# Kernel tuning notes

Hardware: AMD Instinct MI355X
Metric: run time of the kernel (lower is better)

Reference implementation:

```python
import jax, jax.numpy as jnp
import numpy as np

NEG = -1e30  # safe log-space -inf (avoids nan grads from true -inf in logaddexp)


def _ctc_loss(y_true, y_pred):
    """CTC negative log-likelihood per example.

    y_true: [B, L] int labels in [1, C-1] (blank = 0, keras mask_index default)
    y_pred: [B, T, C] logits; input_length = T, label_length = L for all rows
    returns: [B] loss
    """
    B, T, C = y_pred.shape
    L = y_true.shape[1]
    S = 2 * L + 1
    blank = 0
    lp = jax.nn.log_softmax(y_pred, axis=-1)  # [B, T, C]
    # extended label sequence: blank, l1, blank, l2, ..., blank
    ext = jnp.zeros((B, S), dtype=jnp.int32).at[:, 1::2].set(y_true.astype(jnp.int32))
    # log-probs gathered at extended labels: [B, T, S]
    lp_ext = jnp.take_along_axis(lp, jnp.broadcast_to(ext[:, None, :], (B, T, S)), axis=2)
    # skip transition s-2 -> s allowed iff ext[s] is non-blank and differs from ext[s-2]
    can_skip = jnp.zeros((B, S), dtype=bool).at[:, 2:].set(
        (ext[:, 2:] != blank) & (ext[:, 2:] != ext[:, :-2]))
    alpha0 = (jnp.full((B, S), NEG, dtype=lp.dtype)
              .at[:, 0].set(lp_ext[:, 0, 0])
              .at[:, 1].set(lp_ext[:, 0, 1]))

    def step(alpha, lp_t):
        a1 = jnp.pad(alpha, ((0, 0), (1, 0)), constant_values=NEG)[:, :S]  # alpha[s-1]
        a2 = jnp.pad(alpha, ((0, 0), (2, 0)), constant_values=NEG)[:, :S]  # alpha[s-2]
        a2 = jnp.where(can_skip, a2, NEG)
        alpha_new = jnp.logaddexp(jnp.logaddexp(alpha, a1), a2) + lp_t
        return alpha_new, None

    lp_seq = jnp.moveaxis(lp_ext[:, 1:, :], 1, 0)  # [T-1, B, S]
    alphaT, _ = jax.lax.scan(step, alpha0, lp_seq)
    return -jnp.logaddexp(alphaT[:, S - 1], alphaT[:, S - 2])


def setup_inputs() -> dict:
    key = jax.random.key(0)
    k1, k2 = jax.random.split(key)
    B, T, C, L = 2048, 256, 128, 32
    y_pred = jax.random.normal(k1, (B, T, C), dtype=jnp.float32)
    y_true = jax.random.randint(k2, (B, L), 1, C, dtype=jnp.int32)  # avoid blank=0
    return {"y_true": y_true, "y_pred": y_pred}


def reference(y_true, y_pred):
    return _ctc_loss(y_true, y_pred)
```

## Files before the change

### kernel.cpp

```cpp
#include <hip/hip_runtime.h>


__device__ __forceinline__ float dpp_shr1_z(float x) {
    return __int_as_float(__builtin_amdgcn_update_dpp(
        0, __float_as_int(x), 0x138, 0xF, 0xF, false));
}
__device__ __forceinline__ float dpp_bcast_even(float x) {
    return __int_as_float(__builtin_amdgcn_update_dpp(
        0, __float_as_int(x), 0xA0, 0xF, 0xF, true));
}
__device__ __forceinline__ float dpp_mv(float x, int ctrl_is_xor1, int which) {
    return 0.f;
}
__device__ __forceinline__ float dpp_add_xor1(float x) {
    return x + __int_as_float(__builtin_amdgcn_update_dpp(
        0, __float_as_int(x), 0xB1, 0xF, 0xF, true));
}
__device__ __forceinline__ float dpp_add_xor2(float x) {
    return x + __int_as_float(__builtin_amdgcn_update_dpp(
        0, __float_as_int(x), 0x4E, 0xF, 0xF, true));
}
__device__ __forceinline__ float dpp_add_hm(float x) {
    return x + __int_as_float(__builtin_amdgcn_update_dpp(
        0, __float_as_int(x), 0x141, 0xF, 0xF, true));
}
__device__ __forceinline__ float dpp_add_rm(float x) {
    return x + __int_as_float(__builtin_amdgcn_update_dpp(
        0, __float_as_int(x), 0x140, 0xF, 0xF, true));
}
__device__ __forceinline__ float dpp_max_xor1(float x) {
    return fmaxf(x, __int_as_float(__builtin_amdgcn_update_dpp(
        0, __float_as_int(x), 0xB1, 0xF, 0xF, true)));
}
__device__ __forceinline__ float dpp_max_xor2(float x) {
    return fmaxf(x, __int_as_float(__builtin_amdgcn_update_dpp(
        0, __float_as_int(x), 0x4E, 0xF, 0xF, true)));
}
__device__ __forceinline__ float dpp_max_hm(float x) {
    return fmaxf(x, __int_as_float(__builtin_amdgcn_update_dpp(
        0, __float_as_int(x), 0x141, 0xF, 0xF, true)));
}
__device__ __forceinline__ float dpp_max_rm(float x) {
    return fmaxf(x, __int_as_float(__builtin_amdgcn_update_dpp(
        0, __float_as_int(x), 0x140, 0xF, 0xF, true)));
}

__global__ __launch_bounds__(256) void ctc_fused_kernel(
    const int* __restrict__ y_true,
    const float* __restrict__ y_pred,
    float* __restrict__ out)
{
    __shared__ float pstage[8][128];
    __shared__ float pbuf[64][34];
    __shared__ int   labs[32];

    const int tid  = threadIdx.x;
    const int w    = tid >> 6;
    const int lane = tid & 63;
    const int h    = lane >> 5;
    const int l    = lane & 31;
    const int b    = blockIdx.x;

    if (tid < 32) labs[tid] = y_true[b * 32 + tid];
    __syncthreads();

    const float* __restrict__ Y = y_pred + (size_t)b * 256 * 128;

    const int myc   = (l == 0) ? 0 : labs[l - 1];
    const int myc32 = labs[31];

    const int s  = lane;
    const int hi = s >> 1;
    const int li = labs[hi];
    const int lm = (hi >= 1) ? labs[hi - 1] : 0;
    const bool can_skip = (s & 1) && (s >= 3) && (li != lm);
    const int  lpidx    = (s & 1) ? (1 + hi) : 0;

    float alpha = 0.f, a64 = 0.f, shift2 = 0.f;

    float* stg = &pstage[w * 2 + h][0];

    for (int c = 0; c < 4; ++c) {
        for (int it = 0; it < 8; ++it) {
            const int tl = it * 8 + w * 2 + h;
            const int t  = c * 64 + tl;
            const float4 v = ((const float4*)(Y + (size_t)t * 128))[l];
            const float e0 = __expf(v.x), e1 = __expf(v.y);
            const float e2 = __expf(v.z), e3 = __expf(v.w);
            ((float4*)stg)[l] = make_float4(e0, e1, e2, e3);
            float se = (e0 + e1) + (e2 + e3);
            se = dpp_add_xor1(se);
            se = dpp_add_xor2(se);
            se = dpp_add_hm(se);
            se = dpp_add_rm(se);
            se += __shfl_xor(se, 16);
            const float r = __builtin_amdgcn_rcpf(se);
            pbuf[tl][l] = stg[myc] * r;
            if (l == 0) pbuf[tl][32] = stg[myc32] * r;
        }
        __syncthreads();

        if (w == 0) {
            int tl0 = 0;
            if (c == 0) {
                alpha = (s == 0) ? pbuf[0][0] : (s == 1) ? pbuf[0][1] : 0.f;
                tl0 = 1;
            }
            #pragma unroll 4
            for (int tl = tl0; tl < 64; ++tl) {
                const float x  = pbuf[tl][lpidx];
                const float p0 = dpp_bcast_even(x);
                const float a64n = (a64 + alpha) * p0;
                float b1 = dpp_shr1_z(alpha);
                float b2 = dpp_shr1_z(b1);
                b2 = can_skip ? b2 : 0.f;
                alpha = (alpha + b1 + b2) * x;
                a64 = a64n;
                if ((tl & 3) == 3) {
                    float m = alpha;
                    m = dpp_max_xor1(m); m = dpp_max_xor2(m);
                    m = dpp_max_hm(m);   m = dpp_max_rm(m);
                    m = fmaxf(m, __shfl_xor(m, 16));
                    m = fmaxf(m, __shfl_xor(m, 32));
                    const float rr = __builtin_amdgcn_rcpf(m);
                    alpha *= rr;
                    a64   *= rr;
                    shift2 += __log2f(m);
                }
            }
        }
        __syncthreads();
    }

    if (w == 0 && s == 63) {
        out[b] = -((__log2f(alpha + a64) + shift2) * 0.6931471805599453f);
    }
}

extern "C" void kernel_launch(void* const* d_in, const int* in_sizes, int n_in,
                              void* d_out, int out_size, void* d_ws, size_t ws_size,
                              hipStream_t stream) {
    const int*   y_true = (const int*)d_in[0];
    const float* y_pred = (const float*)d_in[1];
    float*       out    = (float*)d_out;
    ctc_fused_kernel<<<2048, 256, 0, stream>>>(y_true, y_pred, out);
}
```

Before: 366.6 us.

## Use single-wave blocks for CTC and replace cross-lane max shuffles with DPP broadcast

```diff
diff --git a/kernel.cpp b/kernel.cpp
--- a/kernel.cpp
+++ b/kernel.cpp
@@ -8,9 +8,6 @@
 __device__ __forceinline__ float dpp_bcast_even(float x) {
     return __int_as_float(__builtin_amdgcn_update_dpp(
         0, __float_as_int(x), 0xA0, 0xF, 0xF, true));
-}
-__device__ __forceinline__ float dpp_mv(float x, int ctrl_is_xor1, int which) {
-    return 0.f;
 }
 __device__ __forceinline__ float dpp_add_xor1(float x) {
     return x + __int_as_float(__builtin_amdgcn_update_dpp(
@@ -44,24 +41,30 @@
     return fmaxf(x, __int_as_float(__builtin_amdgcn_update_dpp(
         0, __float_as_int(x), 0x140, 0xF, 0xF, true)));
 }
+__device__ __forceinline__ float dpp_max_bc15(float x) {
+    return fmaxf(x, __int_as_float(__builtin_amdgcn_update_dpp(
+        0, __float_as_int(x), 0x142, 0xF, 0xF, false)));
+}
+__device__ __forceinline__ float dpp_max_bc31(float x) {
+    return fmaxf(x, __int_as_float(__builtin_amdgcn_update_dpp(
+        0, __float_as_int(x), 0x143, 0xF, 0xF, false)));
+}
 
-__global__ __launch_bounds__(256) void ctc_fused_kernel(
+__global__ __launch_bounds__(64) void ctc_fused_kernel(
     const int* __restrict__ y_true,
     const float* __restrict__ y_pred,
     float* __restrict__ out)
 {
-    __shared__ float pstage[8][128];
+    __shared__ float pstage[4][128];
     __shared__ float pbuf[64][34];
     __shared__ int   labs[32];
 
-    const int tid  = threadIdx.x;
-    const int w    = tid >> 6;
-    const int lane = tid & 63;
+    const int lane = threadIdx.x & 63;
     const int h    = lane >> 5;
     const int l    = lane & 31;
     const int b    = blockIdx.x;
 
-    if (tid < 32) labs[tid] = y_true[b * 32 + tid];
+    if (lane < 32) labs[lane] = y_true[b * 32 + lane];
     __syncthreads();
 
     const float* __restrict__ Y = y_pred + (size_t)b * 256 * 128;
@@ -78,15 +81,15 @@
 
     float alpha = 0.f, a64 = 0.f, shift2 = 0.f;
 
-    float* stg = &pstage[w * 2 + h][0];
-
     for (int c = 0; c < 4; ++c) {
-        for (int it = 0; it < 8; ++it) {
-            const int tl = it * 8 + w * 2 + h;
+        #pragma unroll 4
+        for (int it = 0; it < 32; ++it) {
+            const int tl = it * 2 + h;
             const int t  = c * 64 + tl;
             const float4 v = ((const float4*)(Y + (size_t)t * 128))[l];
             const float e0 = __expf(v.x), e1 = __expf(v.y);
             const float e2 = __expf(v.z), e3 = __expf(v.w);
+            float* stg = &pstage[((it & 1) << 1) + h][0];
             ((float4*)stg)[l] = make_float4(e0, e1, e2, e3);
             float se = (e0 + e1) + (e2 + e3);
             se = dpp_add_xor1(se);
@@ -100,39 +103,38 @@
         }
         __syncthreads();
 
-        if (w == 0) {
-            int tl0 = 0;
-            if (c == 0) {
-                alpha = (s == 0) ? pbuf[0][0] : (s == 1) ? pbuf[0][1] : 0.f;
-                tl0 = 1;
-            }
-            #pragma unroll 4
-            for (int tl = tl0; tl < 64; ++tl) {
-                const float x  = pbuf[tl][lpidx];
-                const float p0 = dpp_bcast_even(x);
-                const float a64n = (a64 + alpha) * p0;
-                float b1 = dpp_shr1_z(alpha);
-                float b2 = dpp_shr1_z(b1);
-                b2 = can_skip ? b2 : 0.f;
-                alpha = (alpha + b1 + b2) * x;
-                a64 = a64n;
-                if ((tl & 3) == 3) {
-                    float m = alpha;
-                    m = dpp_max_xor1(m); m = dpp_max_xor2(m);
-                    m = dpp_max_hm(m);   m = dpp_max_rm(m);
-                    m = fmaxf(m, __shfl_xor(m, 16));
-                    m = fmaxf(m, __shfl_xor(m, 32));
-                    const float rr = __builtin_amdgcn_rcpf(m);
-                    alpha *= rr;
-                    a64   *= rr;
-                    shift2 += __log2f(m);
-                }
+        int tl0 = 0;
+        if (c == 0) {
+            alpha = (s == 0) ? pbuf[0][0] : (s == 1) ? pbuf[0][1] : 0.f;
+            tl0 = 1;
+        }
+        #pragma unroll 4
+        for (int tl = tl0; tl < 64; ++tl) {
+            const float x  = pbuf[tl][lpidx];
+            const float p0 = dpp_bcast_even(x);
+            const float a64n = (a64 + alpha) * p0;
+            float b1 = dpp_shr1_z(alpha);
+            float b2 = dpp_shr1_z(b1);
+            b2 = can_skip ? b2 : 0.f;
+            alpha = (alpha + b1 + b2) * x;
+            a64 = a64n;
+            if ((tl & 3) == 3) {
+                float m = alpha;
+                m = dpp_max_xor1(m); m = dpp_max_xor2(m);
+                m = dpp_max_hm(m);   m = dpp_max_rm(m);
+                m = dpp_max_bc15(m); m = dpp_max_bc31(m);
+                const float mall = __int_as_float(
+                    __builtin_amdgcn_readlane(__float_as_int(m), 63));
+                const float rr = __builtin_amdgcn_rcpf(mall);
+                alpha *= rr;
+                a64   *= rr;
+                shift2 += __log2f(mall);
             }
         }
         __syncthreads();
     }
 
-    if (w == 0 && s == 63) {
+    if (lane == 63) {
         out[b] = -((__log2f(alpha + a64) + shift2) * 0.6931471805599453f);
     }
 }
@@ -143,5 +145,5 @@
     const int*   y_true = (const int*)d_in[0];
     const float* y_pred = (const float*)d_in[1];
     float*       out    = (float*)d_out;
-    ctc_fused_kernel<<<2048, 256, 0, stream>>>(y_true, y_pred, out);
+    ctc_fused_kernel<<<2048, 64, 0, stream>>>(y_true, y_pred, out);
 }
```

After: 403.8 us. 1.1x slower.
